# Optimization experiments

Hardware: AMD Instinct MI355X
Metric: run time of the kernel (lower is better)

Reference implementation:

```python
import jax, jax.numpy as jnp
from jax import lax
import numpy as np

# init_kwargs (FlowNet-C canonical config)
K = 1      # kernel_size
MD = 20    # max_displacement
S1 = 1     # stride_1 (input stride)
S2 = 2     # stride_2 (displacement stride)
PAD = 20   # spatial zero padding


def setup_inputs() -> dict:
    key = jax.random.key(0)
    k1, k2 = jax.random.split(key)
    shape = (16, 48, 64, 256)  # [B, H, W, C], channels_last
    return {
        "input_a": jax.random.normal(k1, shape, dtype=jnp.float32),
        "input_b": jax.random.normal(k2, shape, dtype=jnp.float32),
    }


def _corr(a, b):
    # FlowNet correlation cost volume (TFA addons_correlation_cost semantics).
    B, H, W, C = a.shape
    rad = MD // S2                      # displacement radius in stride_2 steps
    D = 2 * rad + 1                     # displacements per axis
    rk = (K - 1) // 2                   # kernel radius
    bd = MD + rk                        # border
    oH = H + 2 * (PAD - bd) // S1       # matches layer's compute_output_shape
    oW = W + 2 * (PAD - bd) // S1
    rows = (oH - 1) * S1 + K            # extent of input needed (pre-pool)
    cols = (oW - 1) * S1 + K

    pa = jnp.pad(a, ((0, 0), (PAD, PAD), (PAD, PAD), (0, 0)))
    pb = jnp.pad(b, ((0, 0), (PAD, PAD), (PAD, PAD), (0, 0)))
    # static region of A covering all kernel windows (centers at h*S1+bd)
    a_reg = lax.slice(pa, (0, bd - rk, bd - rk, 0),
                      (B, bd - rk + rows, bd - rk + cols, C))

    def body(_, d):
        # top_channel d -> (tj, ti) row-major, tj vertical as in TFA kernel
        dy = (d // D) * S2 - MD
        dx = (d % D) * S2 - MD
        b_reg = lax.dynamic_slice(pb, (0, bd - rk + dy, bd - rk + dx, 0),
                                  (B, rows, cols, C))
        p = jnp.sum(a_reg * b_reg, axis=-1)           # [B, rows, cols]
        o = lax.reduce_window(p, 0.0, lax.add,
                              (1, K, K), (1, S1, S1), 'VALID')  # [B, oH, oW]
        return None, o

    # remat keeps scan residuals small (slices recomputed in any backward pass)
    _, outs = lax.scan(jax.checkpoint(body), None, jnp.arange(D * D))
    # [D*D, B, oH, oW] -> [B, oH, oW, D*D]; TFA kernel divides by K*K*C
    return jnp.transpose(outs, (1, 2, 3, 0)) / (K * K * C)


def reference(input_a, input_b):
    return _corr(input_a, input_b)
```

## Files before the change

kernel.cpp:

```cpp
#include <hip/hip_runtime.h>
#include <hip/hip_bf16.h>

#define HH    48
#define WW    64
#define CC    256
#define ND    21
#define OUTD  441
#define PITCH 264
#define SROWS 32

typedef __bf16 v8bf16 __attribute__((ext_vector_type(8)));
typedef __bf16 v4bf16 __attribute__((ext_vector_type(4)));
typedef float  v4f    __attribute__((ext_vector_type(4)));

__global__ __launch_bounds__(384)
void corr_mfma_kernel(const float* __restrict__ A, const float* __restrict__ B,
                      float* __restrict__ out) {
    __shared__ __bf16 Blds[2][SROWS * PITCH];

    const int blk  = blockIdx.x;
    const int b    = blk >> 5;
    const int rem  = blk & 31;
    const int ck   = rem & 1;
    const int p    = (rem >> 1) & 1;
    const int hpar = (rem >> 2) & 1;
    const int grp  = rem >> 3;
    const int h0   = hpar + 12 * grp;

    const int tid  = threadIdx.x;
    const int lane = tid & 63;
    const int wave = tid >> 6;
    const int mt   = wave & 1;
    const int hg   = wave >> 1;
    const int n    = lane & 15;
    const int quad = lane >> 4;

    const int i_lo_f = (h0 >= 20) ? 0 : ((21 - h0) >> 1);
    const int i_hi_f = min(25, (67 - h0) >> 1);
    const int i_mid  = (i_lo_f + i_hi_f + 1) >> 1;
    const int i_lo   = ck ? i_mid : i_lo_f;
    const int i_hi   = ck ? i_hi_f : (i_mid - 1);

    const float* bimg = B + (size_t)(b * HH) * WW * CC + p * CC;
    float4 pf[6];
    auto load_pf = [&](int hb) {
        const float* brow = bimg + (size_t)hb * WW * CC;
        #pragma unroll
        for (int it = 0; it < 6; ++it) {
            int idx = it * 384 + tid;
            if (idx < 2048)
                pf[it] = *(const float4*)(brow + (idx >> 6) * 2 * CC + ((idx & 63) << 2));
        }
    };
    auto store_lds = [&](int buf) {
        #pragma unroll
        for (int it = 0; it < 6; ++it) {
            int idx = it * 384 + tid;
            if (idx < 2048) {
                v4bf16 t;
                t[0] = (__bf16)pf[it].x; t[1] = (__bf16)pf[it].y;
                t[2] = (__bf16)pf[it].z; t[3] = (__bf16)pf[it].w;
                *(v4bf16*)&Blds[buf][(idx >> 6) * PITCH + ((idx & 63) << 2)] = t;
            }
        }
    };

    load_pf(h0 - 20 + 2 * i_lo);

    for (int r = 0; r < 6; ++r) {
        int z_lo, z_hi;
        if (ck == 0) { z_lo = 0;                      z_hi = min(20, i_lo_f - r - 1); }
        else         { z_lo = max(0, i_hi_f - r + 1); z_hi = 20; }
        if (z_lo > z_hi) continue;
        float* outr = out + (size_t)(b * HH + h0 + 2 * r) * WW * OUTD;
        for (int tj = z_lo; tj <= z_hi; ++tj) {
            for (int idx = tid; idx < 32 * ND; idx += 384) {
                int wp = idx / ND, ti = idx - wp * ND;
                int w  = (wp << 1) + p;
                outr[(size_t)w * OUTD + tj * ND + ti] = 0.f;
            }
        }
    }

    v8bf16 afrag[2][8];
    {
        int w_a = ((mt * 16 + n) << 1) + p;
        #pragma unroll
        for (int rr = 0; rr < 2; ++rr) {
            int h = h0 + 4 * hg + 2 * rr;
            const float* arow = A + ((size_t)(b * HH + h) * WW + w_a) * CC;
            #pragma unroll
            for (int kc = 0; kc < 8; ++kc) {
                int c0 = kc * 32 + quad * 8;
                float4 f0 = *(const float4*)(arow + c0);
                float4 f1 = *(const float4*)(arow + c0 + 4);
                v8bf16 af;
                af[0] = (__bf16)f0.x; af[1] = (__bf16)f0.y; af[2] = (__bf16)f0.z; af[3] = (__bf16)f0.w;
                af[4] = (__bf16)f1.x; af[5] = (__bf16)f1.y; af[6] = (__bf16)f1.z; af[7] = (__bf16)f1.w;
                afrag[rr][kc] = af;
            }
        }
    }

    store_lds(0);
    int cur = 0;

    auto epilogue = [&](const v4f& acc0, const v4f& acc1, int h, int tj) {
        float* outr = out + (size_t)(b * HH + h) * WW * OUTD;
        #pragma unroll
        for (int q = 0; q < 4; ++q) {
            int wp = mt * 16 + quad * 4 + q;
            int w  = (wp << 1) + p;
            float* orow = outr + (size_t)w * OUTD + tj * ND;
            int ti0 = 10 + n - wp;
            if ((unsigned)ti0 < 21u) orow[ti0] = acc0[q] * (1.f / 256.f);
            int ti1 = 26 + n - wp;
            if ((unsigned)ti1 < 21u) orow[ti1] = acc1[q] * (1.f / 256.f);
            if (n < 10 - wp)  orow[n]      = 0.f;
            if (n <= wp - 22) orow[20 - n] = 0.f;
        }
    };

    for (int i = i_lo; i <= i_hi; ++i) {
        if (i < i_hi) load_pf(h0 - 20 + 2 * (i + 1));
        __syncthreads();

        const int tj0 = i - 2 * hg;
        if ((unsigned)tj0 <= 21u) {
            const __bf16* bbase = &Blds[cur][n * PITCH + quad * 8];
            v4f a00 = {0.f, 0.f, 0.f, 0.f};
            v4f a01 = a00, a10 = a00, a11 = a00;
            #pragma unroll
            for (int kc = 0; kc < 8; ++kc) {
                v8bf16 bf0 = *(const v8bf16*)(bbase + kc * 32);
                v8bf16 bf1 = *(const v8bf16*)(bbase + 16 * PITCH + kc * 32);
                a00 = __builtin_amdgcn_mfma_f32_16x16x32_bf16(afrag[0][kc], bf0, a00, 0, 0, 0);
                a01 = __builtin_amdgcn_mfma_f32_16x16x32_bf16(afrag[0][kc], bf1, a01, 0, 0, 0);
                a10 = __builtin_amdgcn_mfma_f32_16x16x32_bf16(afrag[1][kc], bf0, a10, 0, 0, 0);
                a11 = __builtin_amdgcn_mfma_f32_16x16x32_bf16(afrag[1][kc], bf1, a11, 0, 0, 0);
            }
            if ((unsigned)tj0 <= 20u)       epilogue(a00, a01, h0 + 4 * hg,     tj0);
            const int tj1 = tj0 - 1;
            if ((unsigned)tj1 <= 20u)       epilogue(a10, a11, h0 + 4 * hg + 2, tj1);
        }

        if (i < i_hi) store_lds(cur ^ 1);
        cur ^= 1;
    }
}

extern "C" void kernel_launch(void* const* d_in, const int* in_sizes, int n_in,
                              void* d_out, int out_size, void* d_ws, size_t ws_size,
                              hipStream_t stream) {
    const float* A = (const float*)d_in[0];
    const float* B = (const float*)d_in[1];
    float* out = (float*)d_out;
    dim3 grid(16 * 32);
    dim3 block(384);
    corr_mfma_kernel<<<grid, block, 0, stream>>>(A, B, out);
}
```

Before: 206.7 us.

## Stage correlation output in a workspace, then permute with a coalesced pass

The MFMA kernel now writes its results into a workspace laid out by (batch, parity, row, tj, wp, ti), so each tile is written contiguously instead of as scattered 21-float strips with a stride of two output pixels. A second kernel then gathers from the workspace and writes the final NHWC output using float4 stores. This targets poorly coalesced global writes in the main kernel, at the cost of an extra full read and write of the ~87MB output plus a second launch. The new path runs only when a workspace of at least the required size is provided; otherwise the original path is used.

Measured after the change: 224.2 us. +8.5%, slower.

```diff
diff --git a/kernel.cpp b/kernel.cpp
--- a/kernel.cpp
+++ b/kernel.cpp
@@ -9,13 +9,20 @@
 #define PITCH 264
 #define SROWS 32
 
+#define WS_TJ    672
+#define WS_H     14112
+#define WS_P     677376
+#define WS_B     1354752
+#define WS_BYTES (16ull * WS_B * 4ull)
+
 typedef __bf16 v8bf16 __attribute__((ext_vector_type(8)));
 typedef __bf16 v4bf16 __attribute__((ext_vector_type(4)));
 typedef float  v4f    __attribute__((ext_vector_type(4)));
 
+template<bool USE_WS>
 __global__ __launch_bounds__(384)
 void corr_mfma_kernel(const float* __restrict__ A, const float* __restrict__ B,
-                      float* __restrict__ out) {
+                      float* __restrict__ out, float* __restrict__ ws) {
     __shared__ __bf16 Blds[2][SROWS * PITCH];
 
     const int blk  = blockIdx.x;
@@ -41,6 +48,8 @@
     const int i_lo   = ck ? i_mid : i_lo_f;
     const int i_hi   = ck ? i_hi_f : (i_mid - 1);
 
+    float* const wsb = USE_WS ? (ws + (size_t)b * WS_B + (size_t)p * WS_P) : nullptr;
+
     const float* bimg = B + (size_t)(b * HH) * WW * CC + p * CC;
     float4 pf[6];
     auto load_pf = [&](int hb) {
@@ -72,12 +81,18 @@
         if (ck == 0) { z_lo = 0;                      z_hi = min(20, i_lo_f - r - 1); }
         else         { z_lo = max(0, i_hi_f - r + 1); z_hi = 20; }
         if (z_lo > z_hi) continue;
-        float* outr = out + (size_t)(b * HH + h0 + 2 * r) * WW * OUTD;
+        int hrow = h0 + 2 * r;
         for (int tj = z_lo; tj <= z_hi; ++tj) {
-            for (int idx = tid; idx < 32 * ND; idx += 384) {
-                int wp = idx / ND, ti = idx - wp * ND;
-                int w  = (wp << 1) + p;
-                outr[(size_t)w * OUTD + tj * ND + ti] = 0.f;
+            if constexpr (USE_WS) {
+                float* tile = wsb + hrow * WS_H + tj * WS_TJ;
+                for (int idx = tid; idx < WS_TJ; idx += 384) tile[idx] = 0.f;
+            } else {
+                float* outr = out + (size_t)(b * HH + hrow) * WW * OUTD;
+                for (int idx = tid; idx < 32 * ND; idx += 384) {
+                    int wp = idx / ND, ti = idx - wp * ND;
+                    int w  = (wp << 1) + p;
+                    outr[(size_t)w * OUTD + tj * ND + ti] = 0.f;
+                }
             }
         }
     }
@@ -106,18 +121,22 @@
     int cur = 0;
 
     auto epilogue = [&](const v4f& acc0, const v4f& acc1, int h, int tj) {
-        float* outr = out + (size_t)(b * HH + h) * WW * OUTD;
         #pragma unroll
         for (int q = 0; q < 4; ++q) {
             int wp = mt * 16 + quad * 4 + q;
-            int w  = (wp << 1) + p;
-            float* orow = outr + (size_t)w * OUTD + tj * ND;
+            float* strip;
+            if constexpr (USE_WS) {
+                strip = wsb + h * WS_H + tj * WS_TJ + wp * ND;
+            } else {
+                int w = (wp << 1) + p;
+                strip = out + (size_t)(b * HH + h) * WW * OUTD + (size_t)w * OUTD + tj * ND;
+            }
             int ti0 = 10 + n - wp;
-            if ((unsigned)ti0 < 21u) orow[ti0] = acc0[q] * (1.f / 256.f);
+            if ((unsigned)ti0 < 21u) strip[ti0] = acc0[q] * (1.f / 256.f);
             int ti1 = 26 + n - wp;
-            if ((unsigned)ti1 < 21u) orow[ti1] = acc1[q] * (1.f / 256.f);
-            if (n < 10 - wp)  orow[n]      = 0.f;
-            if (n <= wp - 22) orow[20 - n] = 0.f;
+            if ((unsigned)ti1 < 21u) strip[ti1] = acc1[q] * (1.f / 256.f);
+            if (n < 10 - wp)  strip[n]      = 0.f;
+            if (n <= wp - 22) strip[20 - n] = 0.f;
         }
     };
 
@@ -149,13 +168,36 @@
     }
 }
 
+__global__ __launch_bounds__(256)
+void corr_permute_kernel(const float* __restrict__ ws, float* __restrict__ out) {
+    const int bh = blockIdx.x;
+    const int b  = bh / HH, h = bh - b * HH;
+    const float* wsrow = ws + (size_t)b * WS_B + (size_t)h * WS_H;
+    float4* out4 = (float4*)(out + (size_t)bh * (WW * OUTD));
+    for (int idx4 = threadIdx.x; idx4 < (WW * OUTD) / 4; idx4 += 256) {
+        int e = idx4 << 2;
+        float r[4];
+        #pragma unroll
+        for (int k = 0; k < 4; ++k) {
+            int ee = e + k;
+            int w  = ee / OUTD, d = ee - OUTD * w;
+            int tj = d / ND,    ti = d - ND * tj;
+            r[k] = wsrow[(w & 1) * WS_P + tj * WS_TJ + (w >> 1) * ND + ti];
+        }
+        out4[idx4] = make_float4(r[0], r[1], r[2], r[3]);
+    }
+}
+
 extern "C" void kernel_launch(void* const* d_in, const int* in_sizes, int n_in,
                               void* d_out, int out_size, void* d_ws, size_t ws_size,
                               hipStream_t stream) {
     const float* A = (const float*)d_in[0];
     const float* B = (const float*)d_in[1];
     float* out = (float*)d_out;
-    dim3 grid(16 * 32);
-    dim3 block(384);
-    corr_mfma_kernel<<<grid, block, 0, stream>>>(A, B, out);
+    if (ws_size >= WS_BYTES && d_ws != nullptr) {
+        corr_mfma_kernel<true><<<dim3(16 * 32), dim3(384), 0, stream>>>(A, B, out, (float*)d_ws);
+        corr_permute_kernel<<<dim3(16 * HH), dim3(256), 0, stream>>>((const float*)d_ws, out);
+    } else {
+        corr_mfma_kernel<false><<<dim3(16 * 32), dim3(384), 0, stream>>>(A, B, out, nullptr);
+    }
 }
```

## Split correlation into smaller LDS-free workgroups reading B directly

Applied to the files above, without the earlier changes.

Replaces the 384-thread workgroups, which staged B rows through double-buffered LDS with barriers, with 128-thread workgroups that each cover two output rows and load B fragments straight from global memory into MFMA operands. The grid triples to 1536 blocks, and a blockIdx swizzle spreads neighbouring work across XCDs. Zero-fill of the out-of-range displacement rows is reworked per wave. This removes LDS traffic and synchronisation and raises parallelism, but each B row is now re-read from global/L2 by more workgroups and converted to bf16 redundantly.

New measurement: 282.6 us. 1.37x slower.

```diff
diff --git a/kernel.cpp b/kernel.cpp
--- a/kernel.cpp
+++ b/kernel.cpp
@@ -6,80 +6,50 @@
 #define CC    256
 #define ND    21
 #define OUTD  441
-#define PITCH 264
-#define SROWS 32
 
 typedef __bf16 v8bf16 __attribute__((ext_vector_type(8)));
-typedef __bf16 v4bf16 __attribute__((ext_vector_type(4)));
 typedef float  v4f    __attribute__((ext_vector_type(4)));
 
-__global__ __launch_bounds__(384)
+__global__ __launch_bounds__(128)
 void corr_mfma_kernel(const float* __restrict__ A, const float* __restrict__ B,
                       float* __restrict__ out) {
-    __shared__ __bf16 Blds[2][SROWS * PITCH];
-
-    const int blk  = blockIdx.x;
-    const int b    = blk >> 5;
-    const int rem  = blk & 31;
-    const int ck   = rem & 1;
-    const int p    = (rem >> 1) & 1;
-    const int hpar = (rem >> 2) & 1;
-    const int grp  = rem >> 3;
-    const int h0   = hpar + 12 * grp;
+    const int bid = blockIdx.x;
+    const int wg  = (bid & 7) * 192 + (bid >> 3);
+    const int b   = wg / 96;
+    const int r   = wg - b * 96;
+    const int ck  = r & 1;
+    const int p   = (r >> 1) & 1;
+    const int hp  = r >> 2;
+    const int h0  = (hp & 1) + 4 * (hp >> 1);
 
     const int tid  = threadIdx.x;
     const int lane = tid & 63;
-    const int wave = tid >> 6;
-    const int mt   = wave & 1;
-    const int hg   = wave >> 1;
+    const int mt   = tid >> 6;
     const int n    = lane & 15;
     const int quad = lane >> 4;
 
-    const int i_lo_f = (h0 >= 20) ? 0 : ((21 - h0) >> 1);
-    const int i_hi_f = min(25, (67 - h0) >> 1);
-    const int i_mid  = (i_lo_f + i_hi_f + 1) >> 1;
-    const int i_lo   = ck ? i_mid : i_lo_f;
-    const int i_hi   = ck ? i_hi_f : (i_mid - 1);
+    const int I_lo = (h0 >= 20) ? 0 : ((21 - h0) >> 1);
+    const int I_hi = min(21, (67 - h0) >> 1);
+    const int i_mid = (I_lo + I_hi + 1) >> 1;
+    const int i_beg = ck ? i_mid : I_lo;
+    const int i_end = ck ? I_hi : (i_mid - 1);
 
-    const float* bimg = B + (size_t)(b * HH) * WW * CC + p * CC;
-    float4 pf[6];
-    auto load_pf = [&](int hb) {
-        const float* brow = bimg + (size_t)hb * WW * CC;
-        #pragma unroll
-        for (int it = 0; it < 6; ++it) {
-            int idx = it * 384 + tid;
-            if (idx < 2048)
-                pf[it] = *(const float4*)(brow + (idx >> 6) * 2 * CC + ((idx & 63) << 2));
-        }
-    };
-    auto store_lds = [&](int buf) {
-        #pragma unroll
-        for (int it = 0; it < 6; ++it) {
-            int idx = it * 384 + tid;
-            if (idx < 2048) {
-                v4bf16 t;
-                t[0] = (__bf16)pf[it].x; t[1] = (__bf16)pf[it].y;
-                t[2] = (__bf16)pf[it].z; t[3] = (__bf16)pf[it].w;
-                *(v4bf16*)&Blds[buf][(idx >> 6) * PITCH + ((idx & 63) << 2)] = t;
-            }
-        }
-    };
-
-    load_pf(h0 - 20 + 2 * i_lo);
-
-    for (int r = 0; r < 6; ++r) {
-        int z_lo, z_hi;
-        if (ck == 0) { z_lo = 0;                      z_hi = min(20, i_lo_f - r - 1); }
-        else         { z_lo = max(0, i_hi_f - r + 1); z_hi = 20; }
-        if (z_lo > z_hi) continue;
-        float* outr = out + (size_t)(b * HH + h0 + 2 * r) * WW * OUTD;
-        for (int tj = z_lo; tj <= z_hi; ++tj) {
-            for (int idx = tid; idx < 32 * ND; idx += 384) {
-                int wp = idx / ND, ti = idx - wp * ND;
-                int w  = (wp << 1) + p;
+    auto zero_tj = [&](int h, int z_lo, int z_hi) {
+        if (z_lo > z_hi) return;
+        float* outr = out + (size_t)(b * HH + h) * WW * OUTD;
+        for (int tj = z_lo; tj <= z_hi; ++tj)
+            for (int idx = lane; idx < 16 * ND; idx += 64) {
+                int wl = idx / ND, ti = idx - wl * ND;
+                int w  = ((mt * 16 + wl) << 1) + p;
                 outr[(size_t)w * OUTD + tj * ND + ti] = 0.f;
             }
-        }
+    };
+    if (ck == 0) {
+        zero_tj(h0,     0, I_lo - 1);
+        zero_tj(h0 + 2, 0, max(0, I_lo - 1) - 1);
+    } else {
+        zero_tj(h0,     min(20, I_hi) + 1,     20);
+        zero_tj(h0 + 2, min(20, I_hi - 1) + 1, 20);
     }
 
     v8bf16 afrag[2][8];
@@ -87,8 +57,7 @@
         int w_a = ((mt * 16 + n) << 1) + p;
         #pragma unroll
         for (int rr = 0; rr < 2; ++rr) {
-            int h = h0 + 4 * hg + 2 * rr;
-            const float* arow = A + ((size_t)(b * HH + h) * WW + w_a) * CC;
+            const float* arow = A + ((size_t)(b * HH + h0 + 2 * rr) * WW + w_a) * CC;
             #pragma unroll
             for (int kc = 0; kc < 8; ++kc) {
                 int c0 = kc * 32 + quad * 8;
@@ -101,9 +70,6 @@
             }
         }
     }
-
-    store_lds(0);
-    int cur = 0;
 
     auto epilogue = [&](const v4f& acc0, const v4f& acc1, int h, int tj) {
         float* outr = out + (size_t)(b * HH + h) * WW * OUTD;
@@ -121,31 +87,34 @@
         }
     };
 
-    for (int i = i_lo; i <= i_hi; ++i) {
-        if (i < i_hi) load_pf(h0 - 20 + 2 * (i + 1));
-        __syncthreads();
+    const float* bimg = B + (size_t)(b * HH) * WW * CC;
 
-        const int tj0 = i - 2 * hg;
-        if ((unsigned)tj0 <= 21u) {
-            const __bf16* bbase = &Blds[cur][n * PITCH + quad * 8];
-            v4f a00 = {0.f, 0.f, 0.f, 0.f};
-            v4f a01 = a00, a10 = a00, a11 = a00;
-            #pragma unroll
-            for (int kc = 0; kc < 8; ++kc) {
-                v8bf16 bf0 = *(const v8bf16*)(bbase + kc * 32);
-                v8bf16 bf1 = *(const v8bf16*)(bbase + 16 * PITCH + kc * 32);
-                a00 = __builtin_amdgcn_mfma_f32_16x16x32_bf16(afrag[0][kc], bf0, a00, 0, 0, 0);
-                a01 = __builtin_amdgcn_mfma_f32_16x16x32_bf16(afrag[0][kc], bf1, a01, 0, 0, 0);
-                a10 = __builtin_amdgcn_mfma_f32_16x16x32_bf16(afrag[1][kc], bf0, a10, 0, 0, 0);
-                a11 = __builtin_amdgcn_mfma_f32_16x16x32_bf16(afrag[1][kc], bf1, a11, 0, 0, 0);
-            }
-            if ((unsigned)tj0 <= 20u)       epilogue(a00, a01, h0 + 4 * hg,     tj0);
-            const int tj1 = tj0 - 1;
-            if ((unsigned)tj1 <= 20u)       epilogue(a10, a11, h0 + 4 * hg + 2, tj1);
+    for (int i = i_beg; i <= i_end; ++i) {
+        const int hb = h0 - 20 + 2 * i;
+        const float* brow = bimg + ((size_t)hb * WW + p) * CC;
+        const float* bl = brow + (size_t)(2 * n) * CC + quad * 8;
+        const float* bh = brow + (size_t)(2 * (16 + n)) * CC + quad * 8;
+
+        v4f a00 = {0.f, 0.f, 0.f, 0.f};
+        v4f a01 = a00, a10 = a00, a11 = a00;
+        #pragma unroll
+        for (int kc = 0; kc < 8; ++kc) {
+            float4 f0 = *(const float4*)(bl + kc * 32);
+            float4 f1 = *(const float4*)(bl + kc * 32 + 4);
+            float4 g0 = *(const float4*)(bh + kc * 32);
+            float4 g1 = *(const float4*)(bh + kc * 32 + 4);
+            v8bf16 bf0, bf1;
+            bf0[0] = (__bf16)f0.x; bf0[1] = (__bf16)f0.y; bf0[2] = (__bf16)f0.z; bf0[3] = (__bf16)f0.w;
+            bf0[4] = (__bf16)f1.x; bf0[5] = (__bf16)f1.y; bf0[6] = (__bf16)f1.z; bf0[7] = (__bf16)f1.w;
+            bf1[0] = (__bf16)g0.x; bf1[1] = (__bf16)g0.y; bf1[2] = (__bf16)g0.z; bf1[3] = (__bf16)g0.w;
+            bf1[4] = (__bf16)g1.x; bf1[5] = (__bf16)g1.y; bf1[6] = (__bf16)g1.z; bf1[7] = (__bf16)g1.w;
+            a00 = __builtin_amdgcn_mfma_f32_16x16x32_bf16(afrag[0][kc], bf0, a00, 0, 0, 0);
+            a01 = __builtin_amdgcn_mfma_f32_16x16x32_bf16(afrag[0][kc], bf1, a01, 0, 0, 0);
+            a10 = __builtin_amdgcn_mfma_f32_16x16x32_bf16(afrag[1][kc], bf0, a10, 0, 0, 0);
+            a11 = __builtin_amdgcn_mfma_f32_16x16x32_bf16(afrag[1][kc], bf1, a11, 0, 0, 0);
         }
-
-        if (i < i_hi) store_lds(cur ^ 1);
-        cur ^= 1;
+        if (i <= 20) epilogue(a00, a01, h0,     i);
+        if (i >= 1)  epilogue(a10, a11, h0 + 2, i - 1);
     }
 }
 
@@ -155,7 +124,7 @@
     const float* A = (const float*)d_in[0];
     const float* B = (const float*)d_in[1];
     float* out = (float*)d_out;
-    dim3 grid(16 * 32);
-    dim3 block(384);
+    dim3 grid(1536);
+    dim3 block(128);
     corr_mfma_kernel<<<grid, block, 0, stream>>>(A, B, out);
 }
```
